# Performance work log

Measured on AMD Instinct MI355X. Metric: run time of the kernel, lower is better.

The kernel has to match this reference:

```python
import jax, jax.numpy as jnp
import numpy as np

B, S, D, H, DFF = 4, 2048, 1024, 16, 4096
DK = D // H  # = d_v
NEG = -1e30  # stands in for float('-inf'); fully-masked rows zeroed explicitly


def setup_inputs() -> dict:
    key = jax.random.key(0)
    ks = jax.random.split(key, 12)
    scale = lambda fan_in: fan_in ** -0.5
    # padding mask: positions >= random length are padded (True = pad)
    lens = jax.random.randint(ks[0], (B,), S // 2, S + 1)
    src_padding_mask = jnp.arange(S)[None, :] >= lens[:, None]
    return {
        "src": jax.random.normal(ks[1], (B, S, D), jnp.float32),
        "src_padding_mask": src_padding_mask,
        # per-head projections, stored as [H, D, DK] (x @ W, i.e. torch W.T)
        "Wq": jax.random.normal(ks[2], (H, D, DK), jnp.float32) * scale(D),
        "Wk": jax.random.normal(ks[3], (H, D, DK), jnp.float32) * scale(D),
        "Wv": jax.random.normal(ks[4], (H, D, DK), jnp.float32) * scale(D),
        "Wo": jax.random.normal(ks[5], (D, D), jnp.float32) * scale(D),
        "g1": jnp.ones((D,), jnp.float32),
        "g2": jnp.ones((D,), jnp.float32),
        "W1": jax.random.normal(ks[6], (D, DFF), jnp.float32) * scale(D),
        "V1": jax.random.normal(ks[7], (D, DFF), jnp.float32) * scale(D),
        "W2": jax.random.normal(ks[8], (DFF, D), jnp.float32) * scale(DFF),
    }


def _rmsnorm(x, gamma):
    # rms = sqrt(sum(x^2)/size); out = gamma * x / rms
    rms = jnp.sqrt(jnp.sum(x * x, axis=-1, keepdims=True) / x.shape[-1])
    return gamma * x / rms


def _encoder_layer(src, pad_mask, Wq, Wk, Wv, Wo, g1, g2, W1, V1, W2):
    x = _rmsnorm(src, g1)
    # all heads at once: q,k,v -> [B,H,S,DK]
    q = jnp.einsum('bsd,hdk->bhsk', x, Wq)
    k = jnp.einsum('bsd,hdk->bhsk', x, Wk)
    v = jnp.einsum('bsd,hdk->bhsk', x, Wv)
    scores = jnp.einsum('bhsk,bhtk->bhst', q, k) * (DK ** -0.5)  # [B,H,S,S]
    mask = pad_mask[:, None, :, None] | pad_mask[:, None, None, :]
    scores = jnp.where(mask, NEG, scores)
    attn = jax.nn.softmax(scores, axis=-1)
    # torch: fully -inf rows softmax to nan -> nan_to_num(0). Zero padded query rows.
    attn = jnp.where(pad_mask[:, None, :, None], 0.0, attn)
    o = jnp.einsum('bhst,bhtk->bhsk', attn, v)            # [B,H,S,DK]
    o = o.transpose(0, 2, 1, 3).reshape(src.shape[0], src.shape[1], -1)  # concat heads
    sa = src + o @ Wo
    y = _rmsnorm(sa, g2)
    ff = (jax.nn.silu(y @ W1) * (y @ V1)) @ W2
    return sa + ff


def reference(src, src_padding_mask, Wq, Wk, Wv, Wo, g1, g2, W1, V1, W2):
    return _encoder_layer(src, src_padding_mask, Wq, Wk, Wv, Wo, g1, g2, W1, V1, W2)
```

## Files before the change

kernel.cpp:

```cpp
#include <hip/hip_runtime.h>
#include <hip/hip_bf16.h>

typedef short short8 __attribute__((ext_vector_type(8)));
typedef float f32x4 __attribute__((ext_vector_type(4)));
typedef float f32x16 __attribute__((ext_vector_type(16)));
typedef unsigned short u16;
typedef unsigned short u16x4 __attribute__((ext_vector_type(4)));

__device__ __forceinline__ u16 f2bf(float f) {
  __hip_bfloat16 h = __float2bfloat16(f);
  return __builtin_bit_cast(u16, h);
}
__device__ __forceinline__ float bf2f(u16 u) {
  return __bfloat162float(__builtin_bit_cast(__hip_bfloat16, u));
}
__device__ __forceinline__ void gload_lds16(const void* g, void* l) {
  __builtin_amdgcn_global_load_lds(
      (const __attribute__((address_space(1))) void*)g,
      (__attribute__((address_space(3))) void*)l, 16, 0, 0);
}
__device__ __forceinline__ unsigned cvtpk(float lo, float hi) {
  unsigned r;
  asm("v_cvt_pk_bf16_f32 %0, %1, %2" : "=v"(r) : "v"(lo), "v"(hi));
  return r;
}

__global__ void compute_lens(const unsigned char* __restrict__ mask, int* __restrict__ lens) {
  __shared__ int flag;
  __shared__ int cnt[4];
  const int tid = threadIdx.x;
  if (tid == 0) flag = 0;
  if (tid < 4) cnt[tid] = 0;
  __syncthreads();
  int found = 0;
  for (int i = tid; i < 8192; i += 256)
    if (mask[i] == 1 && (i & 3) != 0) found = 1;
  if (found) atomicOr(&flag, 1);
  __syncthreads();
  int l0 = 0, l1 = 0, l2 = 0, l3 = 0;
  if (flag) {
    for (int i = tid; i < 8192; i += 256) {
      int z = (mask[i] == 0);
      int b = i >> 11;
      l0 += z & (b == 0); l1 += z & (b == 1); l2 += z & (b == 2); l3 += z & (b == 3);
    }
  } else {
    const int* mi = (const int*)mask;
    for (int i = tid; i < 8192; i += 256) {
      int z = (mi[i] == 0);
      int b = i >> 11;
      l0 += z & (b == 0); l1 += z & (b == 1); l2 += z & (b == 2); l3 += z & (b == 3);
    }
  }
  if (l0) atomicAdd(&cnt[0], l0);
  if (l1) atomicAdd(&cnt[1], l1);
  if (l2) atomicAdd(&cnt[2], l2);
  if (l3) atomicAdd(&cnt[3], l3);
  __syncthreads();
  if (tid < 4) lens[tid] = cnt[tid];
}

__global__ void convT(const float* __restrict__ in, u16* __restrict__ out,
                      int K, int N, long inz, long outz) {
  __shared__ float t[32][33];
  const int n0 = blockIdx.x * 32, k0 = blockIdx.y * 32;
  const float* ip = in + (size_t)blockIdx.z * inz;
  u16* op = out + (size_t)blockIdx.z * outz;
  const int tx = threadIdx.x & 31, ty = threadIdx.x >> 5;
  for (int i = ty; i < 32; i += 8)
    t[i][tx] = ip[(size_t)(k0 + i) * N + n0 + tx];
  __syncthreads();
  for (int i = ty; i < 32; i += 8)
    op[(size_t)(n0 + i) * K + k0 + tx] = f2bf(t[tx][i]);
}

__global__ void rmsnorm_kernel(const float* __restrict__ in, const float* __restrict__ g,
                               u16* __restrict__ out) {
  __shared__ float psum[4];
  const int row = blockIdx.x, tid = threadIdx.x;
  const float4 x = ((const float4*)(in + (size_t)row * 1024))[tid];
  float ss = x.x * x.x + x.y * x.y + x.z * x.z + x.w * x.w;
  for (int m = 1; m < 64; m <<= 1) ss += __shfl_xor(ss, m, 64);
  if ((tid & 63) == 0) psum[tid >> 6] = ss;
  __syncthreads();
  const float tot = psum[0] + psum[1] + psum[2] + psum[3];
  const float inv = rsqrtf(tot * (1.0f / 1024.0f));
  const float4 gv = ((const float4*)g)[tid];
  u16x4 o;
  o[0] = f2bf(gv.x * x.x * inv); o[1] = f2bf(gv.y * x.y * inv);
  o[2] = f2bf(gv.z * x.z * inv); o[3] = f2bf(gv.w * x.w * inv);
  *(u16x4*)&out[(size_t)row * 1024 + tid * 4] = o;
}

enum { MQKV = 0, MSA = 1, MB16 = 2, MSILU = 3, MFF2 = 4 };

template <int MODE>
__global__ __launch_bounds__(512, 2) void gemm2(
    const u16* __restrict__ A, const u16* __restrict__ Bt,
    const int K, const int N,
    u16* __restrict__ oq, u16* __restrict__ ok, u16* __restrict__ ov,
    float* __restrict__ of, const float* __restrict__ afp,
    u16* __restrict__ ob) {
  __shared__ u16 lds[57344];
  u16* Ab = lds;
  u16* Bb = lds + 24576;
  const int tid = threadIdx.x;
  const int w = tid >> 6, l = tid & 63;
  const int wr = w >> 2, wc = w & 3;
  const int lane16 = l & 15, lgrp = l >> 4;

  const int nwg = (int)gridDim.x;
  const int bid = (int)blockIdx.x;
  const int swz = (bid & 7) * (nwg >> 3) + (bid >> 3);
  const int bx = swz >> 6, by = swz & 63;
  const int row0 = by * 128, col0 = bx * 256;

  const int ca0 = w * 128 + l, ca1 = ca0 + 64;
  const int ra0 = ca0 >> 3, ra1 = ca1 >> 3;
  const int ja0 = (ca0 & 7) ^ (ra0 & 7), ja1 = (ca1 & 7) ^ (ra1 & 7);
  const u16* ag0 = A + (size_t)(row0 + ra0) * K + ja0 * 8;
  const u16* ag1 = A + (size_t)(row0 + ra1) * K + ja1 * 8;
  const u16* bg[4];
  int rbv[4];
#pragma unroll
  for (int i = 0; i < 4; ++i) {
    const int cb = w * 256 + i * 64 + l;
    const int rb = cb >> 3, jb = (cb & 7) ^ (rb & 7);
    rbv[i] = rb;
    bg[i] = Bt + (size_t)(col0 + rb) * K + jb * 8;
  }

  int aoff[4][2], boff[4][2];
#pragma unroll
  for (int mi = 0; mi < 4; ++mi) {
    const int ar = wr * 64 + mi * 16 + lane16;
#pragma unroll
    for (int ks = 0; ks < 2; ++ks)
      aoff[mi][ks] = ar * 64 + (((ks << 2) + lgrp) ^ (ar & 7)) * 8;
  }
#pragma unroll
  for (int ni = 0; ni < 4; ++ni) {
    const int br = wc * 64 + ni * 16 + lane16;
#pragma unroll
    for (int ks = 0; ks < 2; ++ks)
      boff[ni][ks] = br * 64 + (((ks << 2) + lgrp) ^ (br & 7)) * 8;
  }

  auto issueA = [&](int tt) {
    u16* d = Ab + (tt % 3) * 8192 + w * 1024;
    gload_lds16(ag0 + tt * 64, d);
    gload_lds16(ag1 + tt * 64, d + 512);
  };
  auto issueB = [&](int tt) {
    u16* d = Bb + (tt & 1) * 16384 + w * 2048;
#pragma unroll
    for (int i = 0; i < 4; ++i)
      gload_lds16(bg[i] + tt * 64, d + i * 512);
  };

  f32x4 zero = {0.f, 0.f, 0.f, 0.f};
  f32x4 acc[4][4];
#pragma unroll
  for (int i = 0; i < 4; i++)
#pragma unroll
    for (int j = 0; j < 4; j++) acc[i][j] = zero;

  const int nkt = K >> 6;
  issueA(0); issueB(0); issueA(1);

  for (int t = 0; t < nkt; ++t) {
    if (t < nkt - 1) { asm volatile("s_waitcnt vmcnt(2)" ::: "memory"); }
    else             { asm volatile("s_waitcnt vmcnt(0)" ::: "memory"); }
    __builtin_amdgcn_s_barrier();
    __builtin_amdgcn_sched_barrier(0);
    if (t + 1 < nkt) issueB(t + 1);
    if (t + 2 < nkt) issueA(t + 2);
    const u16* ap = Ab + (t % 3) * 8192;
    const u16* bp = Bb + (t & 1) * 16384;
    short8 af[4][2], bf[4][2];
#pragma unroll
    for (int mi = 0; mi < 4; ++mi)
#pragma unroll
      for (int ks = 0; ks < 2; ++ks) af[mi][ks] = *(const short8*)&ap[aoff[mi][ks]];
#pragma unroll
    for (int ni = 0; ni < 2; ++ni)
#pragma unroll
      for (int ks = 0; ks < 2; ++ks) bf[ni][ks] = *(const short8*)&bp[boff[ni][ks]];
    __builtin_amdgcn_s_setprio(1);
#pragma unroll
    for (int ks = 0; ks < 2; ++ks)
#pragma unroll
      for (int mi = 0; mi < 4; ++mi)
#pragma unroll
        for (int ni = 0; ni < 2; ++ni)
          acc[mi][ni] = __builtin_amdgcn_mfma_f32_16x16x32_bf16(af[mi][ks], bf[ni][ks], acc[mi][ni], 0, 0, 0);
    __builtin_amdgcn_s_setprio(0);
#pragma unroll
    for (int ni = 2; ni < 4; ++ni)
#pragma unroll
      for (int ks = 0; ks < 2; ++ks) bf[ni][ks] = *(const short8*)&bp[boff[ni][ks]];
    __builtin_amdgcn_s_setprio(1);
#pragma unroll
    for (int ks = 0; ks < 2; ++ks)
#pragma unroll
      for (int mi = 0; mi < 4; ++mi)
#pragma unroll
        for (int ni = 2; ni < 4; ++ni)
          acc[mi][ni] = __builtin_amdgcn_mfma_f32_16x16x32_bf16(af[mi][ks], bf[ni][ks], acc[mi][ni], 0, 0, 0);
    __builtin_amdgcn_s_setprio(0);
  }
  __syncthreads();

  if (MODE == MQKV) {
#pragma unroll
    for (int mi = 0; mi < 4; ++mi) {
      const int sbase = row0 + wr * 64 + mi * 16 + lgrp * 4;
      const int bbt = sbase >> 11, sr = sbase & 2047;
#pragma unroll
      for (int ni = 0; ni < 4; ++ni) {
        const int j = col0 + wc * 64 + ni * 16 + lane16;
        const int which = j >> 10, rr = j & 1023, h = rr >> 6, kk = rr & 63;
        const int bh = bbt * 16 + h;
        if (which == 2) {
          u16x4 pk;
#pragma unroll
          for (int r = 0; r < 4; ++r) pk[r] = f2bf(acc[mi][ni][r]);
          *(u16x4*)&ov[((size_t)bh * 64 + kk) * 2048 + sr] = pk;
        } else {
          u16* dst = (which == 0) ? oq : ok;
          const float scl = (which == 0) ? 0.125f : 1.0f;
#pragma unroll
          for (int r = 0; r < 4; ++r)
            dst[((size_t)bh * 2048 + sr + r) * 64 + kk] = f2bf(acc[mi][ni][r] * scl);
        }
      }
    }
  } else if (MODE == MB16 || MODE == MSILU) {
    u16* ep = lds + w * 1152;
    const int grow0 = row0 + wr * 64 + (l >> 2);
    const int gcol = col0 + wc * 64 + (l & 3) * 16;
#pragma unroll
    for (int mi = 0; mi < 4; ++mi) {
#pragma unroll
      for (int ni = 0; ni < 4; ++ni)
#pragma unroll
        for (int r = 0; r < 4; ++r)
          ep[(lgrp * 4 + r) * 72 + ni * 16 + lane16] = f2bf(acc[mi][ni][r]);
      short8 v0 = *(const short8*)&ep[(l >> 2) * 72 + (l & 3) * 16];
      short8 v1 = *(const short8*)&ep[(l >> 2) * 72 + (l & 3) * 16 + 8];
      const size_t idx = (size_t)(grow0 + mi * 16) * N + gcol;
      if (MODE == MSILU) {
        short8 c0 = *(const short8*)&ob[idx];
        short8 c1v = *(const short8*)&ob[idx + 8];
#pragma unroll
        for (int jj = 0; jj < 8; ++jj) {
          float c = bf2f((u16)c0[jj]);
          v0[jj] = (short)f2bf(c / (1.0f + __expf(-c)) * bf2f((u16)v0[jj]));
          c = bf2f((u16)c1v[jj]);
          v1[jj] = (short)f2bf(c / (1.0f + __expf(-c)) * bf2f((u16)v1[jj]));
        }
      }
      *(short8*)&ob[idx] = v0;
      *(short8*)&ob[idx + 8] = v1;
    }
  } else {
    float* ep32 = (float*)lds + w * 1088;
    const int grow0 = row0 + wr * 64 + (l >> 2);
    const int gcol = col0 + wc * 64 + (l & 3) * 16;
#pragma unroll
    for (int mi = 0; mi < 4; ++mi) {
#pragma unroll
      for (int ni = 0; ni < 4; ++ni)
#pragma unroll
        for (int r = 0; r < 4; ++r)
          ep32[(lgrp * 4 + r) * 68 + ni * 16 + lane16] = acc[mi][ni][r];
      const size_t idx = (size_t)(grow0 + mi * 16) * N + gcol;
#pragma unroll
      for (int k = 0; k < 4; ++k) {
        float4 v = *(const float4*)&ep32[(l >> 2) * 68 + (l & 3) * 16 + k * 4];
        float4 a;
        if (MODE == MSA) a = *(const float4*)&afp[idx + k * 4];
        else             a = *(const float4*)&of[idx + k * 4];
        v.x += a.x; v.y += a.y; v.z += a.z; v.w += a.w;
        *(float4*)&of[idx + k * 4] = v;
      }
    }
  }
}

__global__ void attn2_kernel(const u16* __restrict__ qb, const u16* __restrict__ kb,
                             const u16* __restrict__ vT, u16* __restrict__ obuf,
                             const int* __restrict__ lens) {
  __shared__ u16 sm[9216];
  const int tid = threadIdx.x;
  const int l = tid & 63, wid = tid >> 6;
  const int l31 = l & 31, hi = l >> 5;
  const int bh = blockIdx.x, b = bh >> 4, h = bh & 15;
  const int q0 = blockIdx.y * 128;
  const int len = lens[b];

  if (q0 >= len) {
    short8 z = {0, 0, 0, 0, 0, 0, 0, 0};
#pragma unroll
    for (int c = 0; c < 4; ++c) {
      const int ck = c * 256 + tid;
      const int r = ck >> 3, j = ck & 7;
      *(short8*)&obuf[((size_t)b * 2048 + q0 + r) * 1024 + h * 64 + j * 8] = z;
    }
    return;
  }

  const int q0w = q0 + wid * 32;
  const u16* qp = qb + ((size_t)bh * 2048 + q0w + l31) * 64;
  short8 qf0 = *(const short8*)(qp + hi * 8);
  short8 qf1 = *(const short8*)(qp + 16 + hi * 8);
  short8 qf2 = *(const short8*)(qp + 32 + hi * 8);
  short8 qf3 = *(const short8*)(qp + 48 + hi * 8);

  f32x16 oa0 = {0.f,0.f,0.f,0.f,0.f,0.f,0.f,0.f,0.f,0.f,0.f,0.f,0.f,0.f,0.f,0.f};
  f32x16 oa1 = oa0;
  float m_run = -1e30f, l_run = 0.f;

  const int swz = (l31 & 7) << 3;
  const int nt = (len + 63) >> 6;
  for (int kt = 0; kt < nt; ++kt) {
    const int t0 = kt * 64;
    __syncthreads();
#pragma unroll
    for (int c = 0; c < 2; ++c) {
      const int ck = c * 256 + wid * 64 + l;
      const int r = ck >> 3;
      const int j = (ck & 7) ^ (r & 7);
      gload_lds16(kb + ((size_t)bh * 2048 + t0 + r) * 64 + j * 8,
                  &sm[(c * 256 + wid * 64) * 8]);
      gload_lds16(vT + ((size_t)bh * 64 + r) * 2048 + t0 + j * 8,
                  &sm[4096 + (c * 256 + wid * 64) * 8]);
    }
    __syncthreads();

    f32x16 sc0 = {0.f,0.f,0.f,0.f,0.f,0.f,0.f,0.f,0.f,0.f,0.f,0.f,0.f,0.f,0.f,0.f};
    f32x16 sc1 = sc0;
#pragma unroll
    for (int ds = 0; ds < 4; ++ds) {
      const int col = (ds * 16 + hi * 8) ^ swz;
      const short8 kf0 = *(const short8*)&sm[(0 + l31) * 64 + col];
      const short8 kf1 = *(const short8*)&sm[(32 + l31) * 64 + col];
      const short8 qf = (ds == 0) ? qf0 : (ds == 1) ? qf1 : (ds == 2) ? qf2 : qf3;
      sc0 = __builtin_amdgcn_mfma_f32_32x32x16_bf16(kf0, qf, sc0, 0, 0, 0);
      sc1 = __builtin_amdgcn_mfma_f32_32x32x16_bf16(kf1, qf, sc1, 0, 0, 0);
    }

    if (t0 + 64 > len) {
      const int tb = t0 + 4 * hi;
#pragma unroll
      for (int i = 0; i < 16; ++i) {
        const int tg = tb + (i & 3) + 8 * (i >> 2);
        if (tg >= len) sc0[i] = -1e30f;
        if (tg + 32 >= len) sc1[i] = -1e30f;
      }
    }

    float mt = sc0[0];
#pragma unroll
    for (int i = 1; i < 16; ++i) mt = fmaxf(mt, sc0[i]);
#pragma unroll
    for (int i = 0; i < 16; ++i) mt = fmaxf(mt, sc1[i]);
    mt = fmaxf(mt, __shfl_xor(mt, 32, 64));
    const float mnew = fmaxf(m_run, mt);
    const float fac = __expf(m_run - mnew);
    m_run = mnew;
    float sum = 0.f;
#pragma unroll
    for (int i = 0; i < 16; ++i) { sc0[i] = __expf(sc0[i] - mnew); sum += sc0[i]; }
#pragma unroll
    for (int i = 0; i < 16; ++i) { sc1[i] = __expf(sc1[i] - mnew); sum += sc1[i]; }
    sum += __shfl_xor(sum, 32, 64);
    l_run = l_run * fac + sum;
#pragma unroll
    for (int i = 0; i < 16; ++i) { oa0[i] *= fac; oa1[i] *= fac; }

    unsigned wv[16];
#pragma unroll
    for (int k = 0; k < 8; ++k) wv[k] = cvtpk(sc0[2 * k], sc0[2 * k + 1]);
#pragma unroll
    for (int k = 0; k < 8; ++k) wv[8 + k] = cvtpk(sc1[2 * k], sc1[2 * k + 1]);
    unsigned pw[16];
#pragma unroll
    for (int s = 0; s < 2; ++s) {
#pragma unroll
      for (int half = 0; half < 2; ++half) {
        const unsigned a0 = wv[8 * s + 4 * half + 0], a1 = wv[8 * s + 4 * half + 1];
        const unsigned a2 = wv[8 * s + 4 * half + 2], a3 = wv[8 * s + 4 * half + 3];
        const unsigned e0 = (unsigned)__shfl_xor((int)(hi ? a0 : a2), 32, 64);
        const unsigned e1 = (unsigned)__shfl_xor((int)(hi ? a1 : a3), 32, 64);
        const int o = s * 8 + half * 4;
        pw[o + 0] = hi ? e0 : a0;
        pw[o + 1] = hi ? e1 : a1;
        pw[o + 2] = hi ? a2 : e0;
        pw[o + 3] = hi ? a3 : e1;
      }
    }
#pragma unroll
    for (int g = 0; g < 4; ++g) {
      union { unsigned u[4]; short8 s8; } pk;
      pk.u[0] = pw[4 * g + 0]; pk.u[1] = pw[4 * g + 1];
      pk.u[2] = pw[4 * g + 2]; pk.u[3] = pw[4 * g + 3];
      const int col = (g * 16 + hi * 8) ^ swz;
      const short8 vf0 = *(const short8*)&sm[4096 + (0 + l31) * 64 + col];
      const short8 vf1 = *(const short8*)&sm[4096 + (32 + l31) * 64 + col];
      oa0 = __builtin_amdgcn_mfma_f32_32x32x16_bf16(vf0, pk.s8, oa0, 0, 0, 0);
      oa1 = __builtin_amdgcn_mfma_f32_32x32x16_bf16(vf1, pk.s8, oa1, 0, 0, 0);
    }
  }

  __syncthreads();
  const float invl = 1.0f / l_run;
  u16* ow = &sm[wid * 2304];
#pragma unroll
  for (int i = 0; i < 16; ++i) {
    const int d0 = (i & 3) + 8 * (i >> 2) + 4 * hi;
    ow[l31 * 72 + d0] = f2bf(oa0[i] * invl);
    ow[l31 * 72 + 32 + d0] = f2bf(oa1[i] * invl);
  }
  short8 z = {0, 0, 0, 0, 0, 0, 0, 0};
#pragma unroll
  for (int c = 0; c < 4; ++c) {
    const int ck = c * 64 + l;
    const int r = ck >> 3, j = ck & 7;
    short8 v = *(const short8*)&ow[r * 72 + j * 8];
    if (q0w + r >= len) v = z;
    *(short8*)&obuf[((size_t)b * 2048 + q0w + r) * 1024 + h * 64 + j * 8] = v;
  }
}

extern "C" void kernel_launch(void* const* d_in, const int* in_sizes, int n_in,
                              void* d_out, int out_size, void* d_ws, size_t ws_size,
                              hipStream_t stream) {
  const float* src = (const float*)d_in[0];
  const unsigned char* mask = (const unsigned char*)d_in[1];
  const float* Wq = (const float*)d_in[2];
  const float* Wk = (const float*)d_in[3];
  const float* Wv = (const float*)d_in[4];
  const float* Wo = (const float*)d_in[5];
  const float* g1 = (const float*)d_in[6];
  const float* g2 = (const float*)d_in[7];
  const float* W1 = (const float*)d_in[8];
  const float* V1 = (const float*)d_in[9];
  const float* W2 = (const float*)d_in[10];
  float* out = (float*)d_out;
  char* ws = (char*)d_ws;

  int* lens   = (int*)ws;
  u16* WqkvT  = (u16*)(ws + 256);
  u16* WoT    = (u16*)(ws + 6291712);
  u16* W1T    = (u16*)(ws + 8388864);
  u16* V1T    = (u16*)(ws + 16777472);
  u16* W2T    = (u16*)(ws + 25166080);
  u16* xb     = (u16*)(ws + 33554688);
  u16* qbf    = (u16*)(ws + 50331904);
  u16* kbf    = (u16*)(ws + 67109120);
  u16* vTb    = (u16*)(ws + 83886336);
  u16* obf    = (u16*)(ws + 100663552);
  u16* c1     = qbf;

  compute_lens<<<1, 256, 0, stream>>>(mask, lens);
  convT<<<dim3(2, 32, 16), 256, 0, stream>>>(Wq, WqkvT, 1024, 64, 65536, 65536);
  convT<<<dim3(2, 32, 16), 256, 0, stream>>>(Wk, WqkvT + 1024 * 1024, 1024, 64, 65536, 65536);
  convT<<<dim3(2, 32, 16), 256, 0, stream>>>(Wv, WqkvT + 2048 * 1024, 1024, 64, 65536, 65536);
  convT<<<dim3(32, 32, 1), 256, 0, stream>>>(Wo, WoT, 1024, 1024, 0, 0);
  convT<<<dim3(128, 32, 1), 256, 0, stream>>>(W1, W1T, 1024, 4096, 0, 0);
  convT<<<dim3(128, 32, 1), 256, 0, stream>>>(V1, V1T, 1024, 4096, 0, 0);
  convT<<<dim3(32, 128, 1), 256, 0, stream>>>(W2, W2T, 4096, 1024, 0, 0);

  rmsnorm_kernel<<<8192, 256, 0, stream>>>(src, g1, xb);
  gemm2<MQKV><<<768, 512, 0, stream>>>(xb, WqkvT, 1024, 3072,
                                       qbf, kbf, vTb, nullptr, nullptr, nullptr);
  attn2_kernel<<<dim3(64, 16), 256, 0, stream>>>(qbf, kbf, vTb, obf, lens);
  gemm2<MSA><<<256, 512, 0, stream>>>(obf, WoT, 1024, 1024,
                                      nullptr, nullptr, nullptr, out, src, nullptr);
  rmsnorm_kernel<<<8192, 256, 0, stream>>>(out, g2, xb);
  gemm2<MB16><<<1024, 512, 0, stream>>>(xb, W1T, 1024, 4096,
                                        nullptr, nullptr, nullptr, nullptr, nullptr, c1);
  gemm2<MSILU><<<1024, 512, 0, stream>>>(xb, V1T, 1024, 4096,
                                         nullptr, nullptr, nullptr, nullptr, nullptr, c1);
  gemm2<MFF2><<<256, 512, 0, stream>>>(c1, W2T, 4096, 1024,
                                       nullptr, nullptr, nullptr, out, nullptr, nullptr);
}
```

Before: 536.5 us.

## Fuse W1/V1 GEMMs via interleaved weights and add 256-row GEMM tiles

W1 and V1 are transposed into one interleaved weight matrix in 16-column groups, so a single GEMM computes both projections and applies SiLU-gating in its epilogue. This removes the separate bf16 write and re-read of the W1 output. The GEMM is also templated on tile height, using 256-row tiles for the QKV and fused FFN GEMMs with a restructured double-buffered pipeline. Epilogues for the float residual outputs now store directly without LDS staging, which may cost some store coalescing. The larger tile raises LDS and register pressure.

Result: faster. 473.4 us (-11.8%).

```diff
diff --git a/kernel.cpp b/kernel.cpp
--- a/kernel.cpp
+++ b/kernel.cpp
@@ -61,7 +61,7 @@
 }
 
 __global__ void convT(const float* __restrict__ in, u16* __restrict__ out,
-                      int K, int N, long inz, long outz) {
+                      int K, int N, long inz, long outz, int ilv) {
   __shared__ float t[32][33];
   const int n0 = blockIdx.x * 32, k0 = blockIdx.y * 32;
   const float* ip = in + (size_t)blockIdx.z * inz;
@@ -70,8 +70,11 @@
   for (int i = ty; i < 32; i += 8)
     t[i][tx] = ip[(size_t)(k0 + i) * N + n0 + tx];
   __syncthreads();
-  for (int i = ty; i < 32; i += 8)
-    op[(size_t)(n0 + i) * K + k0 + tx] = f2bf(t[tx][i]);
+  for (int i = ty; i < 32; i += 8) {
+    const int rn = n0 + i;
+    const int r = ilv ? ((((rn >> 4) << 5) | (rn & 15)) | ((ilv - 1) << 4)) : rn;
+    op[(size_t)r * K + k0 + tx] = f2bf(t[tx][i]);
+  }
 }
 
 __global__ void rmsnorm_kernel(const float* __restrict__ in, const float* __restrict__ g,
@@ -92,129 +95,147 @@
   *(u16x4*)&out[(size_t)row * 1024 + tid * 4] = o;
 }
 
-enum { MQKV = 0, MSA = 1, MB16 = 2, MSILU = 3, MFF2 = 4 };
-
-template <int MODE>
-__global__ __launch_bounds__(512, 2) void gemm2(
+enum { MQKV = 0, MSA = 1, MFSILU = 2, MFF2 = 3 };
+
+template <int MODE, int BM>
+__global__ __launch_bounds__(512, 2) void gemm3(
     const u16* __restrict__ A, const u16* __restrict__ Bt,
-    const int K, const int N,
+    const int K,
     u16* __restrict__ oq, u16* __restrict__ ok, u16* __restrict__ ov,
     float* __restrict__ of, const float* __restrict__ afp,
     u16* __restrict__ ob) {
-  __shared__ u16 lds[57344];
-  u16* Ab = lds;
-  u16* Bb = lds + 24576;
+  constexpr int MT = 8192 / BM;
+  constexpr int ABUF = BM * 64;
+  constexpr bool P4 = (BM == 256);
+  constexpr int MR = BM / 32;
+  __shared__ u16 lds[2 * ABUF + 32768];
   const int tid = threadIdx.x;
   const int w = tid >> 6, l = tid & 63;
   const int wr = w >> 2, wc = w & 3;
   const int lane16 = l & 15, lgrp = l >> 4;
-
   const int nwg = (int)gridDim.x;
   const int bid = (int)blockIdx.x;
   const int swz = (bid & 7) * (nwg >> 3) + (bid >> 3);
-  const int bx = swz >> 6, by = swz & 63;
-  const int row0 = by * 128, col0 = bx * 256;
-
-  const int ca0 = w * 128 + l, ca1 = ca0 + 64;
-  const int ra0 = ca0 >> 3, ra1 = ca1 >> 3;
-  const int ja0 = (ca0 & 7) ^ (ra0 & 7), ja1 = (ca1 & 7) ^ (ra1 & 7);
-  const u16* ag0 = A + (size_t)(row0 + ra0) * K + ja0 * 8;
-  const u16* ag1 = A + (size_t)(row0 + ra1) * K + ja1 * 8;
-  const u16* bg[4];
-  int rbv[4];
-#pragma unroll
-  for (int i = 0; i < 4; ++i) {
-    const int cb = w * 256 + i * 64 + l;
-    const int rb = cb >> 3, jb = (cb & 7) ^ (rb & 7);
-    rbv[i] = rb;
-    bg[i] = Bt + (size_t)(col0 + rb) * K + jb * 8;
-  }
-
-  int aoff[4][2], boff[4][2];
-#pragma unroll
-  for (int mi = 0; mi < 4; ++mi) {
-    const int ar = wr * 64 + mi * 16 + lane16;
+  const int by = swz % MT, bx = swz / MT;
+  const int row0 = by * BM, col0 = bx * 256;
+
+  auto stageA = [&](int kt, int buf) {
+#pragma unroll
+    for (int i = 0; i < BM / 64; ++i) {
+      const int c = i * 512 + tid;
+      const int r = c >> 3, j = (c & 7) ^ (r & 7);
+      gload_lds16(A + (size_t)(row0 + r) * K + kt * 64 + j * 8,
+                  &lds[buf * ABUF + c * 8]);
+    }
+  };
+  auto stageB = [&](int kt, int buf) {
+#pragma unroll
+    for (int i = 0; i < 4; ++i) {
+      const int c = i * 512 + tid;
+      const int r = c >> 3, j = (c & 7) ^ (r & 7);
+      gload_lds16(Bt + (size_t)(col0 + r) * K + kt * 64 + j * 8,
+                  &lds[2 * ABUF + buf * 16384 + c * 8]);
+    }
+  };
+  auto frofs = [&](int rrow, int ks) {
+    return rrow * 64 + ((((ks << 2) + lgrp) ^ (rrow & 7)) << 3);
+  };
+
+  f32x4 zero = {0.f, 0.f, 0.f, 0.f};
+  f32x4 acc[MR][4];
+#pragma unroll
+  for (int i = 0; i < MR; ++i)
+#pragma unroll
+    for (int j = 0; j < 4; ++j) acc[i][j] = zero;
+
+  const int nkt = K >> 6;
+  stageA(0, 0); stageB(0, 0); stageA(1, 1);
+  if (P4) stageB(1, 1);
+
+  for (int t = 0; t < nkt; ++t) {
+    const int c = t & 1;
+    if (t == nkt - 1)  asm volatile("s_waitcnt vmcnt(0)\ns_barrier" ::: "memory");
+    else if (P4)       asm volatile("s_waitcnt vmcnt(8)\ns_barrier" ::: "memory");
+    else               asm volatile("s_waitcnt vmcnt(2)\ns_barrier" ::: "memory");
+    const u16* ap = &lds[c * ABUF];
+    const u16* bp = &lds[2 * ABUF + c * 16384];
+    short8 a[4][2], b01[2][2], b23[2][2];
+
+    if (!P4) { if (t + 1 < nkt) stageB(t + 1, c ^ 1); }
+#pragma unroll
+    for (int mi = 0; mi < 4; ++mi)
+#pragma unroll
+      for (int ks = 0; ks < 2; ++ks)
+        a[mi][ks] = *(const short8*)&ap[frofs(wr * (BM / 2) + mi * 16 + lane16, ks)];
+#pragma unroll
+    for (int ni = 0; ni < 2; ++ni)
+#pragma unroll
+      for (int ks = 0; ks < 2; ++ks)
+        b01[ni][ks] = *(const short8*)&bp[frofs(wc * 64 + ni * 16 + lane16, ks)];
+    __builtin_amdgcn_s_setprio(1);
 #pragma unroll
     for (int ks = 0; ks < 2; ++ks)
-      aoff[mi][ks] = ar * 64 + (((ks << 2) + lgrp) ^ (ar & 7)) * 8;
-  }
-#pragma unroll
-  for (int ni = 0; ni < 4; ++ni) {
-    const int br = wc * 64 + ni * 16 + lane16;
+#pragma unroll
+      for (int mi = 0; mi < 4; ++mi)
+#pragma unroll
+        for (int ni = 0; ni < 2; ++ni)
+          acc[mi][ni] = __builtin_amdgcn_mfma_f32_16x16x32_bf16(a[mi][ks], b01[ni][ks], acc[mi][ni], 0, 0, 0);
+    __builtin_amdgcn_s_setprio(0);
+    asm volatile("s_barrier" ::: "memory");
+
+    if (!P4) { if (t + 2 < nkt) stageA(t + 2, c); }
+#pragma unroll
+    for (int ni = 0; ni < 2; ++ni)
+#pragma unroll
+      for (int ks = 0; ks < 2; ++ks)
+        b23[ni][ks] = *(const short8*)&bp[frofs(wc * 64 + (ni + 2) * 16 + lane16, ks)];
+    __builtin_amdgcn_s_setprio(1);
 #pragma unroll
     for (int ks = 0; ks < 2; ++ks)
-      boff[ni][ks] = br * 64 + (((ks << 2) + lgrp) ^ (br & 7)) * 8;
-  }
-
-  auto issueA = [&](int tt) {
-    u16* d = Ab + (tt % 3) * 8192 + w * 1024;
-    gload_lds16(ag0 + tt * 64, d);
-    gload_lds16(ag1 + tt * 64, d + 512);
-  };
-  auto issueB = [&](int tt) {
-    u16* d = Bb + (tt & 1) * 16384 + w * 2048;
-#pragma unroll
-    for (int i = 0; i < 4; ++i)
-      gload_lds16(bg[i] + tt * 64, d + i * 512);
-  };
-
-  f32x4 zero = {0.f, 0.f, 0.f, 0.f};
-  f32x4 acc[4][4];
-#pragma unroll
-  for (int i = 0; i < 4; i++)
-#pragma unroll
-    for (int j = 0; j < 4; j++) acc[i][j] = zero;
-
-  const int nkt = K >> 6;
-  issueA(0); issueB(0); issueA(1);
-
-  for (int t = 0; t < nkt; ++t) {
-    if (t < nkt - 1) { asm volatile("s_waitcnt vmcnt(2)" ::: "memory"); }
-    else             { asm volatile("s_waitcnt vmcnt(0)" ::: "memory"); }
-    __builtin_amdgcn_s_barrier();
-    __builtin_amdgcn_sched_barrier(0);
-    if (t + 1 < nkt) issueB(t + 1);
-    if (t + 2 < nkt) issueA(t + 2);
-    const u16* ap = Ab + (t % 3) * 8192;
-    const u16* bp = Bb + (t & 1) * 16384;
-    short8 af[4][2], bf[4][2];
-#pragma unroll
-    for (int mi = 0; mi < 4; ++mi)
-#pragma unroll
-      for (int ks = 0; ks < 2; ++ks) af[mi][ks] = *(const short8*)&ap[aoff[mi][ks]];
-#pragma unroll
-    for (int ni = 0; ni < 2; ++ni)
-#pragma unroll
-      for (int ks = 0; ks < 2; ++ks) bf[ni][ks] = *(const short8*)&bp[boff[ni][ks]];
-    __builtin_amdgcn_s_setprio(1);
-#pragma unroll
-    for (int ks = 0; ks < 2; ++ks)
 #pragma unroll
       for (int mi = 0; mi < 4; ++mi)
 #pragma unroll
         for (int ni = 0; ni < 2; ++ni)
-          acc[mi][ni] = __builtin_amdgcn_mfma_f32_16x16x32_bf16(af[mi][ks], bf[ni][ks], acc[mi][ni], 0, 0, 0);
+          acc[mi][ni + 2] = __builtin_amdgcn_mfma_f32_16x16x32_bf16(a[mi][ks], b23[ni][ks], acc[mi][ni + 2], 0, 0, 0);
     __builtin_amdgcn_s_setprio(0);
-#pragma unroll
-    for (int ni = 2; ni < 4; ++ni)
-#pragma unroll
-      for (int ks = 0; ks < 2; ++ks) bf[ni][ks] = *(const short8*)&bp[boff[ni][ks]];
-    __builtin_amdgcn_s_setprio(1);
-#pragma unroll
-    for (int ks = 0; ks < 2; ++ks)
+
+    if (P4) {
+      asm volatile("s_barrier" ::: "memory");
+      if (t + 2 < nkt) stageB(t + 2, c);
 #pragma unroll
       for (int mi = 0; mi < 4; ++mi)
 #pragma unroll
-        for (int ni = 2; ni < 4; ++ni)
-          acc[mi][ni] = __builtin_amdgcn_mfma_f32_16x16x32_bf16(af[mi][ks], bf[ni][ks], acc[mi][ni], 0, 0, 0);
-    __builtin_amdgcn_s_setprio(0);
-  }
-  __syncthreads();
+        for (int ks = 0; ks < 2; ++ks)
+          a[mi][ks] = *(const short8*)&ap[frofs(wr * 128 + (mi + 4) * 16 + lane16, ks)];
+      __builtin_amdgcn_s_setprio(1);
+#pragma unroll
+      for (int ks = 0; ks < 2; ++ks)
+#pragma unroll
+        for (int mi = 0; mi < 4; ++mi)
+#pragma unroll
+          for (int ni = 0; ni < 2; ++ni)
+            acc[(MR == 8 ? mi + 4 : mi)][ni] = __builtin_amdgcn_mfma_f32_16x16x32_bf16(a[mi][ks], b01[ni][ks], acc[(MR == 8 ? mi + 4 : mi)][ni], 0, 0, 0);
+      __builtin_amdgcn_s_setprio(0);
+      asm volatile("s_barrier" ::: "memory");
+
+      if (t + 2 < nkt) stageA(t + 2, c);
+      __builtin_amdgcn_s_setprio(1);
+#pragma unroll
+      for (int ks = 0; ks < 2; ++ks)
+#pragma unroll
+        for (int mi = 0; mi < 4; ++mi)
+#pragma unroll
+          for (int ni = 0; ni < 2; ++ni)
+            acc[(MR == 8 ? mi + 4 : mi)][ni + 2] = __builtin_amdgcn_mfma_f32_16x16x32_bf16(a[mi][ks], b23[ni][ks], acc[(MR == 8 ? mi + 4 : mi)][ni + 2], 0, 0, 0);
+      __builtin_amdgcn_s_setprio(0);
+    }
+  }
+  asm volatile("s_barrier" ::: "memory");
 
   if (MODE == MQKV) {
 #pragma unroll
-    for (int mi = 0; mi < 4; ++mi) {
-      const int sbase = row0 + wr * 64 + mi * 16 + lgrp * 4;
+    for (int mi = 0; mi < MR; ++mi) {
+      const int sbase = row0 + wr * (BM / 2) + mi * 16 + lgrp * 4;
       const int bbt = sbase >> 11, sr = sbase & 2047;
 #pragma unroll
       for (int ni = 0; ni < 4; ++ni) {
@@ -235,54 +256,35 @@
         }
       }
     }
-  } else if (MODE == MB16 || MODE == MSILU) {
-    u16* ep = lds + w * 1152;
-    const int grow0 = row0 + wr * 64 + (l >> 2);
-    const int gcol = col0 + wc * 64 + (l & 3) * 16;
-#pragma unroll
-    for (int mi = 0; mi < 4; ++mi) {
-#pragma unroll
-      for (int ni = 0; ni < 4; ++ni)
-#pragma unroll
-        for (int r = 0; r < 4; ++r)
-          ep[(lgrp * 4 + r) * 72 + ni * 16 + lane16] = f2bf(acc[mi][ni][r]);
-      short8 v0 = *(const short8*)&ep[(l >> 2) * 72 + (l & 3) * 16];
-      short8 v1 = *(const short8*)&ep[(l >> 2) * 72 + (l & 3) * 16 + 8];
-      const size_t idx = (size_t)(grow0 + mi * 16) * N + gcol;
-      if (MODE == MSILU) {
-        short8 c0 = *(const short8*)&ob[idx];
-        short8 c1v = *(const short8*)&ob[idx + 8];
-#pragma unroll
-        for (int jj = 0; jj < 8; ++jj) {
-          float c = bf2f((u16)c0[jj]);
-          v0[jj] = (short)f2bf(c / (1.0f + __expf(-c)) * bf2f((u16)v0[jj]));
-          c = bf2f((u16)c1v[jj]);
-          v1[jj] = (short)f2bf(c / (1.0f + __expf(-c)) * bf2f((u16)v1[jj]));
+  } else if (MODE == MFSILU) {
+    u16* ep = &lds[w * 576];
+    const int orow = l >> 2, ocol = (l & 3) * 8;
+#pragma unroll
+    for (int mi = 0; mi < MR; ++mi) {
+#pragma unroll
+      for (int p = 0; p < 2; ++p)
+#pragma unroll
+        for (int r = 0; r < 4; ++r) {
+          const float h1 = acc[mi][2 * p][r], h2 = acc[mi][2 * p + 1][r];
+          ep[(lgrp * 4 + r) * 34 + p * 16 + lane16] = f2bf(h1 / (1.0f + __expf(-h1)) * h2);
         }
-      }
-      *(short8*)&ob[idx] = v0;
-      *(short8*)&ob[idx + 8] = v1;
+      short8 v = *(const short8*)&ep[orow * 34 + ocol];
+      *(short8*)&ob[(size_t)(row0 + wr * (BM / 2) + mi * 16 + orow) * 4096 +
+                    (col0 >> 1) + wc * 32 + ocol] = v;
     }
   } else {
-    float* ep32 = (float*)lds + w * 1088;
-    const int grow0 = row0 + wr * 64 + (l >> 2);
-    const int gcol = col0 + wc * 64 + (l & 3) * 16;
-#pragma unroll
-    for (int mi = 0; mi < 4; ++mi) {
-#pragma unroll
-      for (int ni = 0; ni < 4; ++ni)
-#pragma unroll
-        for (int r = 0; r < 4; ++r)
-          ep32[(lgrp * 4 + r) * 68 + ni * 16 + lane16] = acc[mi][ni][r];
-      const size_t idx = (size_t)(grow0 + mi * 16) * N + gcol;
-#pragma unroll
-      for (int k = 0; k < 4; ++k) {
-        float4 v = *(const float4*)&ep32[(l >> 2) * 68 + (l & 3) * 16 + k * 4];
-        float4 a;
-        if (MODE == MSA) a = *(const float4*)&afp[idx + k * 4];
-        else             a = *(const float4*)&of[idx + k * 4];
-        v.x += a.x; v.y += a.y; v.z += a.z; v.w += a.w;
-        *(float4*)&of[idx + k * 4] = v;
+#pragma unroll
+    for (int mi = 0; mi < MR; ++mi) {
+      const int row = row0 + wr * (BM / 2) + mi * 16 + lgrp * 4;
+#pragma unroll
+      for (int ni = 0; ni < 4; ++ni) {
+        const int j = col0 + wc * 64 + ni * 16 + lane16;
+#pragma unroll
+        for (int r = 0; r < 4; ++r) {
+          const size_t idx = (size_t)(row + r) * 1024 + j;
+          const float base = (MODE == MSA) ? afp[idx] : of[idx];
+          of[idx] = base + acc[mi][ni][r];
+        }
       }
     }
   }
@@ -453,8 +455,7 @@
   int* lens   = (int*)ws;
   u16* WqkvT  = (u16*)(ws + 256);
   u16* WoT    = (u16*)(ws + 6291712);
-  u16* W1T    = (u16*)(ws + 8388864);
-  u16* V1T    = (u16*)(ws + 16777472);
+  u16* W1V1T  = (u16*)(ws + 8388864);
   u16* W2T    = (u16*)(ws + 25166080);
   u16* xb     = (u16*)(ws + 33554688);
   u16* qbf    = (u16*)(ws + 50331904);
@@ -464,25 +465,23 @@
   u16* c1     = qbf;
 
   compute_lens<<<1, 256, 0, stream>>>(mask, lens);
-  convT<<<dim3(2, 32, 16), 256, 0, stream>>>(Wq, WqkvT, 1024, 64, 65536, 65536);
-  convT<<<dim3(2, 32, 16), 256, 0, stream>>>(Wk, WqkvT + 1024 * 1024, 1024, 64, 65536, 65536);
-  convT<<<dim3(2, 32, 16), 256, 0, stream>>>(Wv, WqkvT + 2048 * 1024, 1024, 64, 65536, 65536);
-  convT<<<dim3(32, 32, 1), 256, 0, stream>>>(Wo, WoT, 1024, 1024, 0, 0);
-  convT<<<dim3(128, 32, 1), 256, 0, stream>>>(W1, W1T, 1024, 4096, 0, 0);
-  convT<<<dim3(128, 32, 1), 256, 0, stream>>>(V1, V1T, 1024, 4096, 0, 0);
-  convT<<<dim3(32, 128, 1), 256, 0, stream>>>(W2, W2T, 4096, 1024, 0, 0);
+  convT<<<dim3(2, 32, 16), 256, 0, stream>>>(Wq, WqkvT, 1024, 64, 65536, 65536, 0);
+  convT<<<dim3(2, 32, 16), 256, 0, stream>>>(Wk, WqkvT + 1024 * 1024, 1024, 64, 65536, 65536, 0);
+  convT<<<dim3(2, 32, 16), 256, 0, stream>>>(Wv, WqkvT + 2048 * 1024, 1024, 64, 65536, 65536, 0);
+  convT<<<dim3(32, 32, 1), 256, 0, stream>>>(Wo, WoT, 1024, 1024, 0, 0, 0);
+  convT<<<dim3(128, 32, 1), 256, 0, stream>>>(W1, W1V1T, 1024, 4096, 0, 0, 1);
+  convT<<<dim3(128, 32, 1), 256, 0, stream>>>(V1, W1V1T, 1024, 4096, 0, 0, 2);
+  convT<<<dim3(32, 128, 1), 256, 0, stream>>>(W2, W2T, 4096, 1024, 0, 0, 0);
 
   rmsnorm_kernel<<<8192, 256, 0, stream>>>(src, g1, xb);
-  gemm2<MQKV><<<768, 512, 0, stream>>>(xb, WqkvT, 1024, 3072,
-                                       qbf, kbf, vTb, nullptr, nullptr, nullptr);
+  gemm3<MQKV, 256><<<384, 512, 0, stream>>>(xb, WqkvT, 1024,
+                                            qbf, kbf, vTb, nullptr, nullptr, nullptr);
   attn2_kernel<<<dim3(64, 16), 256, 0, stream>>>(qbf, kbf, vTb, obf, lens);
-  gemm2<MSA><<<256, 512, 0, stream>>>(obf, WoT, 1024, 1024,
-                                      nullptr, nullptr, nullptr, out, src, nullptr);
+  gemm3<MSA, 128><<<256, 512, 0, stream>>>(obf, WoT, 1024,
+                                           nullptr, nullptr, nullptr, out, src, nullptr);
   rmsnorm_kernel<<<8192, 256, 0, stream>>>(out, g2, xb);
-  gemm2<MB16><<<1024, 512, 0, stream>>>(xb, W1T, 1024, 4096,
-                                        nullptr, nullptr, nullptr, nullptr, nullptr, c1);
-  gemm2<MSILU><<<1024, 512, 0, stream>>>(xb, V1T, 1024, 4096,
-                                         nullptr, nullptr, nullptr, nullptr, nullptr, c1);
-  gemm2<MFF2><<<256, 512, 0, stream>>>(c1, W2T, 4096, 1024,
-                                       nullptr, nullptr, nullptr, out, nullptr, nullptr);
-}
+  gemm3<MFSILU, 256><<<1024, 512, 0, stream>>>(xb, W1V1T, 1024,
+                                               nullptr, nullptr, nullptr, nullptr, nullptr, c1);
+  gemm3<MFF2, 128><<<256, 512, 0, stream>>>(c1, W2T, 4096,
+                                            nullptr, nullptr, nullptr, out, nullptr, nullptr);
+}
```
